# Kernel tuning notes

Hardware: AMD Instinct MI355X
Metric: run time of the kernel (lower is better)

The kernel has to match this reference:

```python
import jax, jax.numpy as jnp
import numpy as np

B, S, F, H = 4, 1024, 256, 8
SCALE = float(F) ** 0.5  # source MULTIPLIES logits by sqrt(f)


def setup_inputs() -> dict:
    key = jax.random.key(0)
    ks = jax.random.split(key, 5)
    # 0.02 init scale keeps sigmoid logits in a non-saturated range
    return {
        "q_input": jax.random.normal(ks[0], (B, S, F), dtype=jnp.float32),
        "Wq": jax.random.normal(ks[1], (F, F * H), dtype=jnp.float32) * 0.02,
        "Wk": jax.random.normal(ks[2], (F, F * H), dtype=jnp.float32) * 0.02,
        "Wv": jax.random.normal(ks[3], (F, F * H), dtype=jnp.float32) * 0.02,
        "Wo": jax.random.normal(ks[4], (F * H, F), dtype=jnp.float32) * 0.02,
    }


def reference(q_input, Wq, Wk, Wv, Wo):
    b, s, f = q_input.shape
    h = Wq.shape[1] // f
    # kv_input is None in source -> self-attention (kv = q_input)
    q = (q_input.reshape(b * s, f) @ Wq).reshape(b, s, f, h)
    k = (q_input.reshape(b * s, f) @ Wk).reshape(b, s, f, h)
    v = (q_input.reshape(b * s, f) @ Wv).reshape(b, s, f, h)
    qkt = jnp.einsum('bifh,bjfh->bijh', q, k)          # [b, i, j, h]
    attn = jax.nn.sigmoid(qkt * SCALE)                  # sigmoid, NOT softmax
    wv = jnp.einsum('bijh,bjfh->bifh', attn, v)         # [b, i, f, h]
    wv = wv.reshape(b * s, f * h)
    out = jax.nn.relu(wv @ Wo)                          # projection + ReLU
    return out.reshape(b, s, f)
```

## Files before the change

### kernel.cpp

```cpp
#include <hip/hip_runtime.h>
#include <math.h>

#define SQ 1024
#define FQ 256
#define FH 2048

typedef _Float16 f16;
typedef f16  f16x8 __attribute__((ext_vector_type(8)));
typedef f16  f16x4 __attribute__((ext_vector_type(4)));
typedef __fp16 fp16x2 __attribute__((ext_vector_type(2)));
typedef float f32x4 __attribute__((ext_vector_type(4)));
typedef float f32x16 __attribute__((ext_vector_type(16)));
typedef unsigned uint2v __attribute__((ext_vector_type(2)));

#define GLOAD_LDS16(gp, lp) \
    __builtin_amdgcn_global_load_lds((const __attribute__((address_space(1))) void*)(gp), \
                                     (__attribute__((address_space(3))) void*)(lp), 16, 0, 0)

#define SIG16(s) __builtin_amdgcn_rcpf(1.0f + __builtin_amdgcn_exp2f(-23.083120654223414f * (s)))

__global__ __launch_bounds__(256) void prep_kernel(const float* __restrict__ x,
                                                   const float* __restrict__ Wq,
                                                   const float* __restrict__ Wk,
                                                   const float* __restrict__ Wv,
                                                   const float* __restrict__ Wo,
                                                   f16* __restrict__ xh,
                                                   f16* __restrict__ wqT,
                                                   f16* __restrict__ wkT,
                                                   f16* __restrict__ wvT,
                                                   f16* __restrict__ woT) {
    const int z = blockIdx.z;
    if (z == 4) {
        int id = (int)(blockIdx.x * 8 + blockIdx.y);
        int idx = (id * 256 + (int)threadIdx.x) * 8;
        float4 a = *(const float4*)(x + idx);
        float4 b = *(const float4*)(x + idx + 4);
        f16x8 v = {(f16)a.x, (f16)a.y, (f16)a.z, (f16)a.w,
                   (f16)b.x, (f16)b.y, (f16)b.z, (f16)b.w};
        *(f16x8*)(xh + idx) = v;
        return;
    }
    __shared__ f16 T[32][33];
    const int tx = threadIdx.x & 31, ty = threadIdx.x >> 5;
    if (z < 3) {
        const float* W = z == 0 ? Wq : (z == 1 ? Wk : Wv);
        f16* WT        = z == 0 ? wqT : (z == 1 ? wkT : wvT);
        const int n0 = blockIdx.x * 32, k0 = blockIdx.y * 32;
#pragma unroll
        for (int i = 0; i < 4; ++i)
            T[ty + i * 8][tx] = (f16)W[(size_t)(k0 + ty + i * 8) * FH + n0 + tx];
        __syncthreads();
#pragma unroll
        for (int i = 0; i < 4; ++i)
            WT[(size_t)(n0 + ty + i * 8) * FQ + k0 + tx] = T[tx][ty + i * 8];
    } else {
        const int n0 = (blockIdx.x >> 3) * 32;
        const int yy = (blockIdx.x & 7) * 8 + blockIdx.y;
        const int ft = yy >> 3, h = yy & 7;
#pragma unroll
        for (int i = 0; i < 4; ++i) {
            int fl = ty + i * 8;
            T[fl][tx] = (f16)Wo[(size_t)((ft * 32 + fl) * 8 + h) * FQ + n0 + tx];
        }
        __syncthreads();
#pragma unroll
        for (int i = 0; i < 4; ++i)
            woT[(size_t)(n0 + ty + i * 8) * FH + h * 256 + ft * 32 + tx] = T[tx][ty + i * 8];
    }
}

__device__ __forceinline__ void stage_sw64(const f16* __restrict__ G, int ldg,
                                           int row0, int c0, f16* S,
                                           int nrows, int w, int lane) {
    const int rsub = lane >> 3;
    const int g    = (lane & 7) ^ (rsub & 7);
#pragma unroll
    for (int rI = w; rI < (nrows >> 3); rI += 4) {
        GLOAD_LDS16(G + (size_t)(row0 + rI * 8 + rsub) * ldg + c0 + g * 8,
                    S + rI * 512);
    }
}

__device__ __forceinline__ void gemm128_sw(const f16* __restrict__ A, int lda,
                                           const f16* __restrict__ Bt, int ldb,
                                           int kbeg, int kend, f16* As, f16* Bs,
                                           f32x4 acc[4][4], int row0, int col0) {
    const int t = threadIdx.x, lane = t & 63, w = t >> 6;
    const int wr = w >> 1, wc = w & 1;
    const int lrow = lane & 15, quad = lane >> 4;
    for (int k0 = kbeg; k0 < kend; k0 += 64) {
        __syncthreads();
        stage_sw64(A, lda, row0, k0, As, 128, w, lane);
        stage_sw64(Bt, ldb, col0, k0, Bs, 128, w, lane);
        __syncthreads();
#pragma unroll
        for (int kk = 0; kk < 2; ++kk) {
            f16x8 af[4], bf[4];
#pragma unroll
            for (int i = 0; i < 4; ++i) {
                int r = wr * 64 + i * 16 + lrow;
                af[i] = *(const f16x8*)&As[r * 64 + (((kk * 4 + quad) ^ (r & 7)) << 3)];
            }
#pragma unroll
            for (int j = 0; j < 4; ++j) {
                int r = wc * 64 + j * 16 + lrow;
                bf[j] = *(const f16x8*)&Bs[r * 64 + (((kk * 4 + quad) ^ (r & 7)) << 3)];
            }
#pragma unroll
            for (int i = 0; i < 4; ++i)
#pragma unroll
                for (int j = 0; j < 4; ++j)
                    acc[i][j] = __builtin_amdgcn_mfma_f32_16x16x32_f16(af[i], bf[j], acc[i][j], 0, 0, 0);
        }
    }
}

__global__ __launch_bounds__(256) void proj_mfma(const f16* __restrict__ xh,
                                                 const f16* __restrict__ wqT,
                                                 const f16* __restrict__ wkT,
                                                 const f16* __restrict__ wvT,
                                                 f16* __restrict__ qb,
                                                 f16* __restrict__ kb,
                                                 f16* __restrict__ vb) {
    const int z = blockIdx.z;
    const f16* WT = z == 0 ? wqT : (z == 1 ? wkT : wvT);
    f16* O        = z == 0 ? qb  : (z == 1 ? kb  : vb);
    __shared__ f16 smem[17408];
    f16* As = smem;
    f16* Bs = smem + 8192;
    f32x4 acc[4][4] = {};
    const int row0 = blockIdx.y * 128, col0 = blockIdx.x * 128;
    gemm128_sw(xh, FQ, WT, FQ, 0, FQ, As, Bs, acc, row0, col0);

    __syncthreads();
    f16* Es = smem;
    const int lane = threadIdx.x & 63, w = threadIdx.x >> 6;
    const int wr = w >> 1, wc = w & 1;
    const int lrow = lane & 15, quad = lane >> 4;
    if (z != 2) {
#pragma unroll
        for (int i = 0; i < 4; ++i)
#pragma unroll
            for (int rr = 0; rr < 4; ++rr) {
                int rl = 64 * wr + 16 * i + 4 * quad + rr;
#pragma unroll
                for (int j = 0; j < 4; ++j) {
                    int cc = 64 * wc + 16 * j + lrow;
                    Es[rl * 136 + (cc & 7) * 16 + (cc >> 3)] = (f16)acc[i][j][rr];
                }
            }
        __syncthreads();
        const int f0 = col0 >> 3;
#pragma unroll
        for (int it = 0; it < 4; ++it) {
            int c = it * 256 + threadIdx.x;
            int row = c >> 3, hh = c & 7;
            int gr = row0 + row, bbb = gr >> 10, s = gr & 1023;
            f16x8 v0 = *(const f16x8*)&Es[row * 136 + hh * 16];
            f16x8 v1 = *(const f16x8*)&Es[row * 136 + hh * 16 + 8];
            f16* dst = O + ((size_t)(bbb * 8 + hh) * SQ + s) * FQ + f0;
            *(f16x8*)dst = v0;
            *(f16x8*)(dst + 8) = v1;
        }
    } else {
#pragma unroll
        for (int i = 0; i < 4; ++i)
#pragma unroll
            for (int rr = 0; rr < 4; ++rr) {
                int rl = 64 * wr + 16 * i + 4 * quad + rr;
#pragma unroll
                for (int j = 0; j < 4; ++j) {
                    int cc = 64 * wc + 16 * j + lrow;
                    Es[cc * 136 + rl] = (f16)acc[i][j][rr];
                }
            }
        __syncthreads();
        const int bbb = row0 >> 10, s0 = row0 & 1023;
#pragma unroll
        for (int it = 0; it < 8; ++it) {
            int c = it * 256 + threadIdx.x;
            int cc = c >> 4, sc = c & 15;
            int hh = cc & 7, f = (col0 >> 3) + (cc >> 3);
            f16x8 v = *(const f16x8*)&Es[cc * 136 + sc * 8];
            *(f16x8*)(O + ((size_t)(bbb * 8 + hh) * FQ + f) * SQ + s0 + sc * 8) = v;
        }
    }
}

__global__ __launch_bounds__(512, 2) void fused_attn(const f16* __restrict__ Qb,
                                                     const f16* __restrict__ Kb,
                                                     const f16* __restrict__ Vt,
                                                     f16* __restrict__ WV) {
    __shared__ f16 smem[67584];
    const int t = threadIdx.x, lane = t & 63, w = t >> 6;
    const int grp = w >> 2, wl = w & 3;
    const int l31 = lane & 31, hf = lane >> 5;
    const int n = blockIdx.x;
    const int xcd = n & 7, rest = n >> 3;
    const int bh = xcd * 4 + (rest & 3);
    const int strip = rest >> 2;
    const int m0 = strip * 128;
    const int bb = bh >> 3, h = bh & 7;
    const f16* Qg = Qb + (size_t)bh * SQ * FQ;
    const f16* Kg = Kb + (size_t)bh * SQ * FQ;
    const f16* Vg = Vt + (size_t)bh * FQ * SQ;

    f16x8 qf[16];
#pragma unroll
    for (int ks = 0; ks < 16; ++ks)
        qf[ks] = *(const f16x8*)(Qg + (size_t)(m0 + 32 * wl + l31) * FQ + ks * 16 + hf * 8);

    const int krs = lane >> 5;
    const int kgp = lane & 31;
    const int vrs = lane >> 2;
    const int vgp = lane & 3;

    if (grp == 0) {
#pragma unroll
        for (int kt = 0; kt < 2; ++kt)
#pragma unroll
            for (int i = 0; i < 4; ++i) {
                int rI = wl + i * 4;
                int r = rI * 2 + krs;
                GLOAD_LDS16(Kg + (size_t)(kt * 32 + r) * FQ + ((kgp ^ (r & 7)) << 3),
                            smem + kt * 8192 + rI * 512);
            }
    } else {
#pragma unroll
        for (int kt = 0; kt < 2; ++kt)
#pragma unroll
            for (int i = 0; i < 4; ++i) {
                int rI = wl + i * 4;
                int f = rI * 16 + vrs;
                GLOAD_LDS16(Vg + (size_t)f * SQ + kt * 32 + ((vgp ^ ((f >> 1) & 3)) << 3),
                            smem + 32768 + kt * 8192 + rI * 512);
            }
    }

    f32x16 acc_o[8] = {};

    for (int it = 0; it < 16; ++it) {
        const int p = it & 1;
        f16* KBc = smem + (p * 2 + grp) * 8192;
        f16* VBc = smem + 32768 + (p * 2 + grp) * 8192;
        __syncthreads();
        if (it < 15) {
            const int pn = p ^ 1;
            const int base = (it + 1) * 64;
            if (grp == 0) {
#pragma unroll
                for (int kt = 0; kt < 2; ++kt)
#pragma unroll
                    for (int i = 0; i < 4; ++i) {
                        int rI = wl + i * 4;
                        int r = rI * 2 + krs;
                        GLOAD_LDS16(Kg + (size_t)(base + kt * 32 + r) * FQ + ((kgp ^ (r & 7)) << 3),
                                    smem + (pn * 2 + kt) * 8192 + rI * 512);
                    }
            } else {
#pragma unroll
                for (int kt = 0; kt < 2; ++kt)
#pragma unroll
                    for (int i = 0; i < 4; ++i) {
                        int rI = wl + i * 4;
                        int f = rI * 16 + vrs;
                        GLOAD_LDS16(Vg + (size_t)f * SQ + base + kt * 32 + ((vgp ^ ((f >> 1) & 3)) << 3),
                                    smem + 32768 + (pn * 2 + kt) * 8192 + rI * 512);
                    }
            }
        }
        f32x16 acc_s = {};
#pragma unroll
        for (int ks = 0; ks < 16; ++ks) {
            int pg = (2 * ks + hf) ^ (l31 & 7);
            f16x8 af = *(const f16x8*)&KBc[l31 * 256 + (pg << 3)];
            acc_s = __builtin_amdgcn_mfma_f32_32x32x16_f16(af, qf[ks], acc_s, 0, 0, 0);
        }
        f16x8 pa0, pa1;
        {
            unsigned wpk[8];
#pragma unroll
            for (int i = 0; i < 8; ++i) {
                fp16x2 pk = __builtin_amdgcn_cvt_pkrtz(SIG16(acc_s[2 * i]),
                                                       SIG16(acc_s[2 * i + 1]));
                wpk[i] = __builtin_bit_cast(unsigned, pk);
            }
            uint2v r0 = __builtin_amdgcn_permlane32_swap(wpk[0], wpk[2], false, false);
            uint2v r1 = __builtin_amdgcn_permlane32_swap(wpk[1], wpk[3], false, false);
            uint2v r2 = __builtin_amdgcn_permlane32_swap(wpk[4], wpk[6], false, false);
            uint2v r3 = __builtin_amdgcn_permlane32_swap(wpk[5], wpk[7], false, false);
            union { unsigned u[4]; f16x8 v; } u0, u1;
            u0.u[0] = r0[0]; u0.u[1] = r1[0]; u0.u[2] = r0[1]; u0.u[3] = r1[1];
            u1.u[0] = r2[0]; u1.u[1] = r3[0]; u1.u[2] = r2[1]; u1.u[3] = r3[1];
            pa0 = u0.v;
            pa1 = u1.v;
        }
#pragma unroll
        for (int nt = 0; nt < 8; ++nt) {
            int f = 32 * nt + l31;
            int sw = (f >> 1) & 3;
            f16x8 bv0 = *(const f16x8*)&VBc[f * 32 + ((hf ^ sw) << 3)];
            f16x8 bv1 = *(const f16x8*)&VBc[f * 32 + (((2 + hf) ^ sw) << 3)];
            acc_o[nt] = __builtin_amdgcn_mfma_f32_32x32x16_f16(pa0, bv0, acc_o[nt], 0, 0, 0);
            acc_o[nt] = __builtin_amdgcn_mfma_f32_32x32x16_f16(pa1, bv1, acc_o[nt], 0, 0, 0);
        }
    }
    __syncthreads();
    float* Fb = (float*)(smem + 34816);
    f16* Es = smem;
#pragma unroll
    for (int np = 0; np < 2; ++np) {
        if (grp == 1) {
#pragma unroll
            for (int nt4 = 0; nt4 < 4; ++nt4) {
                int nt = np * 4 + nt4;
#pragma unroll
                for (int r2 = 0; r2 < 4; ++r2) {
                    f32x4 c = {acc_o[nt][4 * r2], acc_o[nt][4 * r2 + 1],
                               acc_o[nt][4 * r2 + 2], acc_o[nt][4 * r2 + 3]};
                    *(f32x4*)&Fb[(((wl * 4 + nt4) * 4 + r2) << 8) + lane * 4] = c;
                }
            }
        }
        __syncthreads();
        if (grp == 0) {
#pragma unroll
            for (int nt4 = 0; nt4 < 4; ++nt4) {
                int nt = np * 4 + nt4;
#pragma unroll
                for (int r2 = 0; r2 < 4; ++r2) {
                    f32x4 own = {acc_o[nt][4 * r2], acc_o[nt][4 * r2 + 1],
                                 acc_o[nt][4 * r2 + 2], acc_o[nt][4 * r2 + 3]};
                    f32x4 s = own + *(const f32x4*)&Fb[(((wl * 4 + nt4) * 4 + r2) << 8) + lane * 4];
#pragma unroll
                    for (int rr = 0; rr < 4; ++rr)
                        Es[(32 * wl + rr + 8 * r2 + 4 * hf) * 264 + 32 * nt + l31] =
                            (f16)s[rr];
                }
            }
        }
        __syncthreads();
    }
#pragma unroll
    for (int it = 0; it < 8; ++it) {
        int c = it * 512 + t;
        int r = c >> 5, ck = c & 31;
        f16x8 v = *(const f16x8*)&Es[r * 264 + ck * 8];
        *(f16x8*)(WV + (size_t)(bb * SQ + m0 + r) * FH + h * 256 + ck * 8) = v;
    }
}

__global__ __launch_bounds__(256) void out_mfma4(const f16* __restrict__ WVm,
                                                 const f16* __restrict__ WoT,
                                                 float* __restrict__ PP) {
    __shared__ f16 smem[16384];
    f16* As = smem;
    f16* Bs = smem + 8192;
    f32x4 acc[4][4] = {};
    const int row0 = blockIdx.y * 128, col0 = blockIdx.x * 128;
    const int kbeg = blockIdx.z * 512;
    gemm128_sw(WVm, FH, WoT, FH, kbeg, kbeg + 512, As, Bs, acc, row0, col0);

    float* P = PP + (size_t)blockIdx.z * SQ * 4 * FQ;
    const int lane = threadIdx.x & 63, w = threadIdx.x >> 6;
    const int wr = w >> 1, wc = w & 1;
    const int lrow = lane & 15, quad = lane >> 4;
#pragma unroll
    for (int i = 0; i < 4; ++i)
#pragma unroll
        for (int rr = 0; rr < 4; ++rr) {
            int gr = row0 + wr * 64 + i * 16 + quad * 4 + rr;
#pragma unroll
            for (int j = 0; j < 4; ++j) {
                int gc = col0 + wc * 64 + j * 16 + lrow;
                P[(size_t)gr * FQ + gc] = acc[i][j][rr];
            }
        }
}

__global__ __launch_bounds__(256) void reduce_relu4(const float* __restrict__ PP,
                                                    float* __restrict__ O) {
    int idx = (blockIdx.x * 256 + threadIdx.x) * 4;
    f32x4 s = *(const f32x4*)(PP + idx);
#pragma unroll
    for (int z = 1; z < 4; ++z)
        s += *(const f32x4*)(PP + (size_t)z * 1048576 + idx);
    f32x4 r = {fmaxf(s.x, 0.f), fmaxf(s.y, 0.f), fmaxf(s.z, 0.f), fmaxf(s.w, 0.f)};
    *(f32x4*)(O + idx) = r;
}

extern "C" void kernel_launch(void* const* d_in, const int* in_sizes, int n_in,
                              void* d_out, int out_size, void* d_ws, size_t ws_size,
                              hipStream_t stream) {
    const float* x  = (const float*)d_in[0];
    const float* Wq = (const float*)d_in[1];
    const float* Wk = (const float*)d_in[2];
    const float* Wv = (const float*)d_in[3];
    const float* Wo = (const float*)d_in[4];
    float* out = (float*)d_out;

    f16* ws = (f16*)d_ws;
    f16* xh    = ws;
    f16* wqT   = xh    + 1048576;
    f16* wkT   = wqT   + 524288;
    f16* wvT   = wkT   + 524288;
    f16* woT   = wvT   + 524288;
    f16* qbuf  = woT   + 524288;
    f16* kbuf  = qbuf  + 8388608;
    f16* vbuf  = kbuf  + 8388608;
    f16* wvbuf = vbuf  + 8388608;
    float* pp  = (float*)qbuf;

    dim3 blk(256);
    prep_kernel<<<dim3(64, 8, 5), blk, 0, stream>>>(x, Wq, Wk, Wv, Wo,
                                                    xh, wqT, wkT, wvT, woT);

    proj_mfma<<<dim3(16, 32, 3), blk, 0, stream>>>(xh, wqT, wkT, wvT, qbuf, kbuf, vbuf);

    fused_attn<<<dim3(256), dim3(512), 0, stream>>>(qbuf, kbuf, vbuf, wvbuf);

    out_mfma4<<<dim3(2, 32, 4), blk, 0, stream>>>(wvbuf, woT, pp);
    reduce_relu4<<<dim3(1024), blk, 0, stream>>>(pp, out);
}
```

Baseline: 162.2 us.

## Halve attention block to 64 query rows and drop K/V double buffering

The fused attention kernel now runs 512 blocks of 256 threads (4 waves) with 64 query rows each, instead of 256 blocks of 512 threads with 128 rows. LDS drops to a single buffer of K and V tiles, loaded synchronously after compute with barriers on both sides, in place of the previous double-buffered prefetch. The aim is more resident blocks per CU and finer scheduling granularity. In exchange, global-to-LDS loads are no longer overlapped with MFMA work inside a block, and each K/V tile is fetched by twice as many blocks.

```diff
diff --git a/kernel.cpp b/kernel.cpp
--- a/kernel.cpp
+++ b/kernel.cpp
@@ -187,19 +187,19 @@
     }
 }
 
-__global__ __launch_bounds__(512, 2) void fused_attn(const f16* __restrict__ Qb,
+__global__ __launch_bounds__(256, 2) void fused_attn(const f16* __restrict__ Qb,
                                                      const f16* __restrict__ Kb,
                                                      const f16* __restrict__ Vt,
                                                      f16* __restrict__ WV) {
-    __shared__ f16 smem[67584];
+    __shared__ f16 smem[32768];
     const int t = threadIdx.x, lane = t & 63, w = t >> 6;
-    const int grp = w >> 2, wl = w & 3;
+    const int grp = w >> 1, wl = w & 1;
     const int l31 = lane & 31, hf = lane >> 5;
     const int n = blockIdx.x;
     const int xcd = n & 7, rest = n >> 3;
     const int bh = xcd * 4 + (rest & 3);
     const int strip = rest >> 2;
-    const int m0 = strip * 128;
+    const int m0 = strip * 64;
     const int bb = bh >> 3, h = bh & 7;
     const f16* Qg = Qb + (size_t)bh * SQ * FQ;
     const f16* Kg = Kb + (size_t)bh * SQ * FQ;
@@ -215,60 +215,35 @@
     const int vrs = lane >> 2;
     const int vgp = lane & 3;
 
-    if (grp == 0) {
-#pragma unroll
-        for (int kt = 0; kt < 2; ++kt)
-#pragma unroll
-            for (int i = 0; i < 4; ++i) {
-                int rI = wl + i * 4;
-                int r = rI * 2 + krs;
-                GLOAD_LDS16(Kg + (size_t)(kt * 32 + r) * FQ + ((kgp ^ (r & 7)) << 3),
-                            smem + kt * 8192 + rI * 512);
-            }
-    } else {
-#pragma unroll
-        for (int kt = 0; kt < 2; ++kt)
-#pragma unroll
-            for (int i = 0; i < 4; ++i) {
-                int rI = wl + i * 4;
-                int f = rI * 16 + vrs;
-                GLOAD_LDS16(Vg + (size_t)f * SQ + kt * 32 + ((vgp ^ ((f >> 1) & 3)) << 3),
-                            smem + 32768 + kt * 8192 + rI * 512);
-            }
-    }
+    f16* KBc = smem + grp * 8192;
+    f16* VBc = smem + 16384 + grp * 8192;
+    f16* Sdst = (w < 2) ? (smem + wl * 8192) : (smem + 16384 + wl * 8192);
+
+    auto stage = [&](int it) {
+        const int j0 = it * 64 + wl * 32;
+        if (w < 2) {
+#pragma unroll
+            for (int i = 0; i < 16; ++i) {
+                int r = i * 2 + krs;
+                GLOAD_LDS16(Kg + (size_t)(j0 + r) * FQ + ((kgp ^ (r & 7)) << 3),
+                            Sdst + i * 512);
+            }
+        } else {
+#pragma unroll
+            for (int i = 0; i < 16; ++i) {
+                int f = i * 16 + vrs;
+                GLOAD_LDS16(Vg + (size_t)f * SQ + j0 + ((vgp ^ ((f >> 1) & 3)) << 3),
+                            Sdst + i * 512);
+            }
+        }
+    };
+
+    stage(0);
+    __syncthreads();
 
     f32x16 acc_o[8] = {};
 
     for (int it = 0; it < 16; ++it) {
-        const int p = it & 1;
-        f16* KBc = smem + (p * 2 + grp) * 8192;
-        f16* VBc = smem + 32768 + (p * 2 + grp) * 8192;
-        __syncthreads();
-        if (it < 15) {
-            const int pn = p ^ 1;
-            const int base = (it + 1) * 64;
-            if (grp == 0) {
-#pragma unroll
-                for (int kt = 0; kt < 2; ++kt)
-#pragma unroll
-                    for (int i = 0; i < 4; ++i) {
-                        int rI = wl + i * 4;
-                        int r = rI * 2 + krs;
-                        GLOAD_LDS16(Kg + (size_t)(base + kt * 32 + r) * FQ + ((kgp ^ (r & 7)) << 3),
-                                    smem + (pn * 2 + kt) * 8192 + rI * 512);
-                    }
-            } else {
-#pragma unroll
-                for (int kt = 0; kt < 2; ++kt)
-#pragma unroll
-                    for (int i = 0; i < 4; ++i) {
-                        int rI = wl + i * 4;
-                        int f = rI * 16 + vrs;
-                        GLOAD_LDS16(Vg + (size_t)f * SQ + base + kt * 32 + ((vgp ^ ((f >> 1) & 3)) << 3),
-                                    smem + 32768 + (pn * 2 + kt) * 8192 + rI * 512);
-                    }
-            }
-        }
         f32x16 acc_s = {};
 #pragma unroll
         for (int ks = 0; ks < 16; ++ks) {
@@ -304,34 +279,36 @@
             acc_o[nt] = __builtin_amdgcn_mfma_f32_32x32x16_f16(pa0, bv0, acc_o[nt], 0, 0, 0);
             acc_o[nt] = __builtin_amdgcn_mfma_f32_32x32x16_f16(pa1, bv1, acc_o[nt], 0, 0, 0);
         }
-    }
-    __syncthreads();
-    float* Fb = (float*)(smem + 34816);
+        __syncthreads();
+        if (it < 15) stage(it + 1);
+        __syncthreads();
+    }
+    float* Fb = (float*)(smem + 17408);
     f16* Es = smem;
 #pragma unroll
-    for (int np = 0; np < 2; ++np) {
+    for (int np = 0; np < 4; ++np) {
         if (grp == 1) {
 #pragma unroll
-            for (int nt4 = 0; nt4 < 4; ++nt4) {
-                int nt = np * 4 + nt4;
+            for (int ntl = 0; ntl < 2; ++ntl) {
+                int nt = np * 2 + ntl;
 #pragma unroll
                 for (int r2 = 0; r2 < 4; ++r2) {
                     f32x4 c = {acc_o[nt][4 * r2], acc_o[nt][4 * r2 + 1],
                                acc_o[nt][4 * r2 + 2], acc_o[nt][4 * r2 + 3]};
-                    *(f32x4*)&Fb[(((wl * 4 + nt4) * 4 + r2) << 8) + lane * 4] = c;
+                    *(f32x4*)&Fb[(((wl * 2 + ntl) * 4 + r2) << 8) + lane * 4] = c;
                 }
             }
         }
         __syncthreads();
         if (grp == 0) {
 #pragma unroll
-            for (int nt4 = 0; nt4 < 4; ++nt4) {
-                int nt = np * 4 + nt4;
+            for (int ntl = 0; ntl < 2; ++ntl) {
+                int nt = np * 2 + ntl;
 #pragma unroll
                 for (int r2 = 0; r2 < 4; ++r2) {
                     f32x4 own = {acc_o[nt][4 * r2], acc_o[nt][4 * r2 + 1],
                                  acc_o[nt][4 * r2 + 2], acc_o[nt][4 * r2 + 3]};
-                    f32x4 s = own + *(const f32x4*)&Fb[(((wl * 4 + nt4) * 4 + r2) << 8) + lane * 4];
+                    f32x4 s = own + *(const f32x4*)&Fb[(((wl * 2 + ntl) * 4 + r2) << 8) + lane * 4];
 #pragma unroll
                     for (int rr = 0; rr < 4; ++rr)
                         Es[(32 * wl + rr + 8 * r2 + 4 * hf) * 264 + 32 * nt + l31] =
@@ -343,7 +320,7 @@
     }
 #pragma unroll
     for (int it = 0; it < 8; ++it) {
-        int c = it * 512 + t;
+        int c = it * 256 + t;
         int r = c >> 5, ck = c & 31;
         f16x8 v = *(const f16x8*)&Es[r * 264 + ck * 8];
         *(f16x8*)(WV + (size_t)(bb * SQ + m0 + r) * FH + h * 256 + ck * 8) = v;
@@ -417,7 +394,7 @@
 
     proj_mfma<<<dim3(16, 32, 3), blk, 0, stream>>>(xh, wqT, wkT, wvT, qbuf, kbuf, vbuf);
 
-    fused_attn<<<dim3(256), dim3(512), 0, stream>>>(qbuf, kbuf, vbuf, wvbuf);
+    fused_attn<<<dim3(512), blk, 0, stream>>>(qbuf, kbuf, vbuf, wvbuf);
 
     out_mfma4<<<dim3(2, 32, 4), blk, 0, stream>>>(wvbuf, woT, pp);
     reduce_relu4<<<dim3(1024), blk, 0, stream>>>(pp, out);
```

Result: slower. 187.6 us (+15.7%).

## Double-buffer LDS staging with 32-wide K tiles in projection and output GEMMs

Applied to the files above, without the earlier changes.

Replaces the single-buffered 64-wide K loop of the shared GEMM helper with a double-buffered 32-wide loop. The next tile's async global-to-LDS loads are issued before the MFMAs on the current tile, and only one barrier is used per iteration. The intent is to hide global load latency behind matrix compute in the projection and output kernels. In exchange, K steps are smaller, giving more iterations and barriers, and the LDS swizzle becomes a 4-way XOR pattern that may cause more bank conflicts.

```diff
diff --git a/kernel.cpp b/kernel.cpp
--- a/kernel.cpp
+++ b/kernel.cpp
@@ -69,49 +69,56 @@
     }
 }
 
-__device__ __forceinline__ void stage_sw64(const f16* __restrict__ G, int ldg,
+__device__ __forceinline__ void stage_sw32(const f16* __restrict__ G, int ldg,
                                            int row0, int c0, f16* S,
-                                           int nrows, int w, int lane) {
-    const int rsub = lane >> 3;
-    const int g    = (lane & 7) ^ (rsub & 7);
-#pragma unroll
-    for (int rI = w; rI < (nrows >> 3); rI += 4) {
-        GLOAD_LDS16(G + (size_t)(row0 + rI * 8 + rsub) * ldg + c0 + g * 8,
-                    S + rI * 512);
-    }
-}
-
-__device__ __forceinline__ void gemm128_sw(const f16* __restrict__ A, int lda,
-                                           const f16* __restrict__ Bt, int ldb,
-                                           int kbeg, int kend, f16* As, f16* Bs,
-                                           f32x4 acc[4][4], int row0, int col0) {
+                                           int w, int lane) {
+    const int rsub = lane >> 2;
+    const int gp   = lane & 3;
+#pragma unroll
+    for (int i = 0; i < 2; ++i) {
+        int chunk = i * 4 + w;
+        int r = chunk * 16 + rsub;
+        GLOAD_LDS16(G + (size_t)(row0 + r) * ldg + c0 + ((gp ^ (r & 3)) << 3),
+                    S + chunk * 512);
+    }
+}
+
+__device__ __forceinline__ void gemm128_db32(const f16* __restrict__ A, int lda,
+                                             const f16* __restrict__ Bt, int ldb,
+                                             int kbeg, int kend, f16* smem,
+                                             f32x4 acc[4][4], int row0, int col0) {
     const int t = threadIdx.x, lane = t & 63, w = t >> 6;
     const int wr = w >> 1, wc = w & 1;
     const int lrow = lane & 15, quad = lane >> 4;
-    for (int k0 = kbeg; k0 < kend; k0 += 64) {
-        __syncthreads();
-        stage_sw64(A, lda, row0, k0, As, 128, w, lane);
-        stage_sw64(Bt, ldb, col0, k0, Bs, 128, w, lane);
-        __syncthreads();
-#pragma unroll
-        for (int kk = 0; kk < 2; ++kk) {
-            f16x8 af[4], bf[4];
-#pragma unroll
-            for (int i = 0; i < 4; ++i) {
-                int r = wr * 64 + i * 16 + lrow;
-                af[i] = *(const f16x8*)&As[r * 64 + (((kk * 4 + quad) ^ (r & 7)) << 3)];
-            }
-#pragma unroll
-            for (int j = 0; j < 4; ++j) {
-                int r = wc * 64 + j * 16 + lrow;
-                bf[j] = *(const f16x8*)&Bs[r * 64 + (((kk * 4 + quad) ^ (r & 7)) << 3)];
-            }
-#pragma unroll
-            for (int i = 0; i < 4; ++i)
-#pragma unroll
-                for (int j = 0; j < 4; ++j)
-                    acc[i][j] = __builtin_amdgcn_mfma_f32_16x16x32_f16(af[i], bf[j], acc[i][j], 0, 0, 0);
-        }
+    int cur = 0;
+    stage_sw32(A, lda, row0, kbeg, smem, w, lane);
+    stage_sw32(Bt, ldb, col0, kbeg, smem + 4096, w, lane);
+    for (int k0 = kbeg; k0 < kend; k0 += 32) {
+        f16* As = smem + cur * 8192;
+        f16* Bs = As + 4096;
+        __syncthreads();
+        if (k0 + 32 < kend) {
+            f16* An = smem + (cur ^ 1) * 8192;
+            stage_sw32(A, lda, row0, k0 + 32, An, w, lane);
+            stage_sw32(Bt, ldb, col0, k0 + 32, An + 4096, w, lane);
+        }
+        f16x8 af[4], bf[4];
+#pragma unroll
+        for (int i = 0; i < 4; ++i) {
+            int r = wr * 64 + i * 16 + lrow;
+            af[i] = *(const f16x8*)&As[r * 32 + ((quad ^ (r & 3)) << 3)];
+        }
+#pragma unroll
+        for (int j = 0; j < 4; ++j) {
+            int r = wc * 64 + j * 16 + lrow;
+            bf[j] = *(const f16x8*)&Bs[r * 32 + ((quad ^ (r & 3)) << 3)];
+        }
+#pragma unroll
+        for (int i = 0; i < 4; ++i)
+#pragma unroll
+            for (int j = 0; j < 4; ++j)
+                acc[i][j] = __builtin_amdgcn_mfma_f32_16x16x32_f16(af[i], bf[j], acc[i][j], 0, 0, 0);
+        cur ^= 1;
     }
 }
 
@@ -126,11 +133,9 @@
     const f16* WT = z == 0 ? wqT : (z == 1 ? wkT : wvT);
     f16* O        = z == 0 ? qb  : (z == 1 ? kb  : vb);
     __shared__ f16 smem[17408];
-    f16* As = smem;
-    f16* Bs = smem + 8192;
     f32x4 acc[4][4] = {};
     const int row0 = blockIdx.y * 128, col0 = blockIdx.x * 128;
-    gemm128_sw(xh, FQ, WT, FQ, 0, FQ, As, Bs, acc, row0, col0);
+    gemm128_db32(xh, FQ, WT, FQ, 0, FQ, smem, acc, row0, col0);
 
     __syncthreads();
     f16* Es = smem;
@@ -354,12 +359,10 @@
                                                  const f16* __restrict__ WoT,
                                                  float* __restrict__ PP) {
     __shared__ f16 smem[16384];
-    f16* As = smem;
-    f16* Bs = smem + 8192;
     f32x4 acc[4][4] = {};
     const int row0 = blockIdx.y * 128, col0 = blockIdx.x * 128;
     const int kbeg = blockIdx.z * 512;
-    gemm128_sw(WVm, FH, WoT, FH, kbeg, kbeg + 512, As, Bs, acc, row0, col0);
+    gemm128_db32(WVm, FH, WoT, FH, kbeg, kbeg + 512, smem, acc, row0, col0);
 
     float* P = PP + (size_t)blockIdx.z * SQ * 4 * FQ;
     const int lane = threadIdx.x & 63, w = threadIdx.x >> 6;
```

Result: slower. 166.8 us (+2.8%).
